# Kernel optimization log

Measured on AMD Instinct MI355X. Metric: run time of the kernel, lower is better.

Reference implementation:

```python
import jax, jax.numpy as jnp
import numpy as np

B = 2048          # number of trees (batch)
K = 511           # nodes per complete binary tree (depth 9: levels 0..8)
DEPTH = 9
VOCAB = 200000
EDIM = 128


def setup_inputs() -> dict:
    key = jax.random.key(0)
    k1, k2, k3, k4 = jax.random.split(key, 4)
    N = B * K
    i = np.arange(K)
    lvl = np.floor(np.log2(i + 1)).astype(np.int32)            # level within tree, 0..8
    par_local = np.where(i > 0, (i - 1) // 2, 0).astype(np.int64)  # root points to itself
    offs = (np.arange(B, dtype=np.int64) * K)[:, None]
    parent = jnp.asarray((offs + par_local[None, :]).reshape(-1), dtype=jnp.int32)
    level = jnp.asarray(np.tile(lvl, B), dtype=jnp.int32)
    batch_id = jnp.asarray(np.repeat(np.arange(B, dtype=np.int64), K), dtype=jnp.int32)
    tokens = jax.random.randint(k1, (N,), 0, VOCAB, dtype=jnp.int32)
    emb_weight = jax.random.normal(k2, (VOCAB, EDIM), dtype=jnp.float32) * 0.02
    W = jax.random.normal(k3, (EDIM, EDIM), dtype=jnp.float32) * 0.05
    b = jax.random.normal(k4, (EDIM,), dtype=jnp.float32) * 0.01
    return {"emb_weight": emb_weight, "W": W, "b": b,
            "tokens": tokens, "parent": parent, "level": level, "batch_id": batch_id}


def reference(emb_weight, W, b, tokens, parent, level, batch_id):
    # per-node projection: W_c(embedding(token))  -> [N, EDIM]
    h = emb_weight[tokens] @ W + b
    # bottom-up child aggregation: h[parent] += h[child], deepest level first
    for l in range(DEPTH - 1, 0, -1):
        contrib = jnp.where((level == l)[:, None], h, 0.0)
        h = h.at[parent].add(contrib)
    # torch.max over all node_list snapshots == per-tree elementwise max of node
    # states, clamped at 0 by the zero rows of untouched batch_node snapshots.
    seg_max = jax.ops.segment_max(h, batch_id, num_segments=B)
    return jnp.maximum(seg_max, 0.0)
```

## Files before the change

### kernel.cpp

```cpp
#include <hip/hip_runtime.h>
#include <hip/hip_bf16.h>
#include <stdint.h>

#define VOCAB 200000
#define EDIM 128
#define NTREES 2048
#define KNODES 511

typedef __attribute__((ext_vector_type(4))) float f32x4;
typedef __attribute__((ext_vector_type(2))) float f32x2;
typedef __attribute__((ext_vector_type(8))) short s16x8;
typedef __attribute__((ext_vector_type(8))) unsigned short u16x8;

__device__ __forceinline__ unsigned short f2bf(float x) {
  unsigned u = __builtin_bit_cast(unsigned, x);
  return (unsigned short)((u + 0x7fffu + ((u >> 16) & 1u)) >> 16);
}
__device__ __forceinline__ float bf2f(unsigned short h) {
  unsigned u = ((unsigned)h) << 16;
  return __builtin_bit_cast(float, u);
}

__device__ __forceinline__ unsigned fp8enc(float v) {
  unsigned u = __builtin_bit_cast(unsigned, v);
  unsigned s = (u >> 24) & 0x80u;
  unsigned au = u & 0x7fffffffu;
  au = au > 0x43E00000u ? 0x43E00000u : au;
  unsigned r = au + 0x0007ffffu + ((au >> 20) & 1u);
  unsigned code = (((r >> 23) - 120u) << 3) | ((r >> 20) & 7u);
  float a = __builtin_bit_cast(float, au);
  unsigned sub = (unsigned)(int)rintf(a * 512.0f);
  unsigned c = (au < 0x3C800000u) ? sub : code;
  return c | s;
}
__device__ __forceinline__ float fp8dec(unsigned b) {
  unsigned e = (b >> 3) & 15u, m = b & 7u;
  float n = __builtin_bit_cast(float, ((e + 120u) << 23) | (m << 20));
  float sv = (float)(int)m * 0.001953125f;
  float v = e ? n : sv;
  return (b & 0x80u) ? -v : v;
}

__device__ __forceinline__ unsigned enc4(float a, float b, float c, float d) {
#if __has_builtin(__builtin_amdgcn_cvt_pk_fp8_f32)
  int pk = 0;
  pk = __builtin_amdgcn_cvt_pk_fp8_f32(a, b, pk, false);
  pk = __builtin_amdgcn_cvt_pk_fp8_f32(c, d, pk, true);
  return (unsigned)pk;
#else
  return fp8enc(a) | (fp8enc(b) << 8) | (fp8enc(c) << 16) | (fp8enc(d) << 24);
#endif
}

__device__ __forceinline__ void dec8(uint2 v, float* o) {
#if __has_builtin(__builtin_amdgcn_cvt_pk_f32_fp8)
  f32x2 a = __builtin_amdgcn_cvt_pk_f32_fp8(v.x, false);
  f32x2 b = __builtin_amdgcn_cvt_pk_f32_fp8(v.x, true);
  f32x2 c = __builtin_amdgcn_cvt_pk_f32_fp8(v.y, false);
  f32x2 d = __builtin_amdgcn_cvt_pk_f32_fp8(v.y, true);
  o[0] = a[0]; o[1] = a[1]; o[2] = b[0]; o[3] = b[1];
  o[4] = c[0]; o[5] = c[1]; o[6] = d[0]; o[7] = d[1];
#else
#pragma unroll
  for (int i = 0; i < 4; ++i) o[i] = fp8dec((v.x >> (8 * i)) & 0xFFu);
#pragma unroll
  for (int i = 0; i < 4; ++i) o[4 + i] = fp8dec((v.y >> (8 * i)) & 0xFFu);
#endif
}

__device__ __forceinline__ s16x8 cvt8(f32x4 a, f32x4 b) {
  u16x8 t;
#pragma unroll
  for (int i = 0; i < 4; ++i)
    t[i] = __builtin_bit_cast(unsigned short, __float2bfloat16(a[i]));
#pragma unroll
  for (int i = 0; i < 4; ++i)
    t[4 + i] = __builtin_bit_cast(unsigned short, __float2bfloat16(b[i]));
  return __builtin_bit_cast(s16x8, t);
}

__global__ __launch_bounds__(256) void proj_kernel(
    const float* __restrict__ emb, const float* __restrict__ W,
    const float* __restrict__ bias, unsigned char* __restrict__ T8) {
  __shared__ unsigned short WT[EDIM][136];
  __shared__ float bsh[EDIM];

  const int tid = threadIdx.x;
  for (int idx = tid; idx < EDIM * EDIM; idx += 256) {
    int k = idx >> 7, n = idx & 127;
    WT[n][k] = f2bf(W[idx] * 64.0f);
  }
  if (tid < EDIM) bsh[tid] = bias[tid] * 64.0f;
  __syncthreads();

  const int w = tid >> 6, lane = tid & 63;
  const int q = lane >> 4, cl = lane & 15;
  const long rowbase = (long)blockIdx.x * 128 + (long)w * 32;

  const float* rowp[2];
#pragma unroll
  for (int rt = 0; rt < 2; ++rt) {
    long r = rowbase + rt * 16 + cl;
    if (r >= VOCAB) r = VOCAB - 1;
    rowp[rt] = emb + r * EDIM + q * 8;
  }

  f32x4 acc[2][8];
#pragma unroll
  for (int rt = 0; rt < 2; ++rt)
#pragma unroll
    for (int nt = 0; nt < 8; ++nt) acc[rt][nt] = (f32x4){0.f, 0.f, 0.f, 0.f};

  f32x4 pa[2][2], pb[2][2];
#pragma unroll
  for (int rt = 0; rt < 2; ++rt) {
    pa[0][rt] = *(const f32x4*)(rowp[rt]);
    pb[0][rt] = *(const f32x4*)(rowp[rt] + 4);
  }

#pragma unroll
  for (int ks = 0; ks < 4; ++ks) {
    const int cur = ks & 1, nxt = cur ^ 1;
    if (ks < 3) {
#pragma unroll
      for (int rt = 0; rt < 2; ++rt) {
        pa[nxt][rt] = *(const f32x4*)(rowp[rt] + (ks + 1) * 32);
        pb[nxt][rt] = *(const f32x4*)(rowp[rt] + (ks + 1) * 32 + 4);
      }
    }
    s16x8 ef[2];
#pragma unroll
    for (int rt = 0; rt < 2; ++rt) ef[rt] = cvt8(pa[cur][rt], pb[cur][rt]);

    const int k0 = ks * 32 + q * 8;
#pragma unroll
    for (int nt = 0; nt < 8; ++nt) {
      s16x8 wf = *(const s16x8*)&WT[nt * 16 + cl][k0];
#pragma unroll
      for (int rt = 0; rt < 2; ++rt)
        acc[rt][nt] = __builtin_amdgcn_mfma_f32_16x16x32_bf16(wf, ef[rt], acc[rt][nt], 0, 0, 0);
    }
  }

#pragma unroll
  for (int rt = 0; rt < 2; ++rt) {
    long row = rowbase + rt * 16 + cl;
    if (row < VOCAB) {
#pragma unroll
      for (int nt = 0; nt < 8; ++nt) {
        const int col0 = nt * 16 + q * 4;
        float g0 = acc[rt][nt][0] + bsh[col0 + 0];
        float g1 = acc[rt][nt][1] + bsh[col0 + 1];
        float g2 = acc[rt][nt][2] + bsh[col0 + 2];
        float g3 = acc[rt][nt][3] + bsh[col0 + 3];
        *(unsigned*)&T8[row * EDIM + col0] = enc4(g0, g1, g2, g3);
      }
    }
  }
}

__global__ __launch_bounds__(512, 4) void tree_kernel(
    const unsigned char* __restrict__ T8, const int* __restrict__ tokens,
    float* __restrict__ out) {
  __shared__ unsigned char P8[512][EDIM];
  unsigned char* lds = &P8[0][0];
  const int SOFF = 16384;
  const int MOFF = 53248;

  const int tid = threadIdx.x;
  const int tree = blockIdx.x;
  const int wv = tid >> 6, lane = tid & 63;

  const int* tk = tokens + (long)tree * KNODES;
  int toks[8];
#pragma unroll
  for (int i = 0; i < 8; ++i) {
    int node = wv * 64 + i * 8 + (lane >> 3);
    toks[i] = tk[node > 510 ? 510 : node];
  }
  const int chunk = (lane & 7) ^ ((lane >> 3) & 7);
#pragma unroll
  for (int i = 0; i < 8; ++i) {
    const unsigned char* src = T8 + (long)toks[i] * EDIM + chunk * 16;
    unsigned char* dst = &P8[wv * 64 + i * 8][0];
    __builtin_amdgcn_global_load_lds(
        (const __attribute__((address_space(1))) unsigned int*)src,
        (__attribute__((address_space(3))) unsigned int*)dst, 16, 0, 0);
  }
  __syncthreads();

  auto ldP8 = [&](int row, int q8) -> uint2 {
    int g = q8 >> 1, h = q8 & 1;
    return *(const uint2*)(lds + row * 128 + (((g ^ (row & 7))) << 4) + h * 8);
  };
  auto saddr = [&](int slot, int q16) -> unsigned char* {
    return lds + SOFF + slot * 288 + ((q16 ^ (slot & 7)) << 4);
  };

  const int q = tid & 15;
  const int jg = tid >> 4;
  float rmax[8];
#pragma unroll
  for (int e = 0; e < 8; ++e) rmax[e] = 0.f;

  u16x8 sp7[4];
#pragma unroll
  for (int k = 0; k < 4; ++k) {
    const int p = jg + 32 * k, m = 127 + p;
    uint2 pr = ldP8(m, q);
    uint2 xr = ldP8(2 * m + 1, q);
    uint2 yr = ldP8(2 * m + 2, q);
    float pv[8], xv[8], yv[8];
    dec8(pr, pv); dec8(xr, xv); dec8(yr, yv);
#pragma unroll
    for (int e = 0; e < 8; ++e) {
      float sv = pv[e] + xv[e] + yv[e];
      rmax[e] = fmaxf(rmax[e], fmaxf(fmaxf(xv[e], yv[e]), sv));
      sp7[k][e] = f2bf(sv);
    }
  }
  __syncthreads();
#pragma unroll
  for (int k = 0; k < 4; ++k) *(u16x8*)saddr(jg + 32 * k, q) = sp7[k];
  __syncthreads();

  for (int l = 6; l >= 0; --l) {
    const int cnt = 1 << l;
    for (int p = jg; p < cnt; p += 32) {
      const int m = cnt - 1 + p;
      const int ps = p << (7 - l);
      const int c2s = ps + (1 << (6 - l));
      uint2 pr = ldP8(m, q);
      u16x8 c1 = *(const u16x8*)saddr(ps, q);
      u16x8 c2 = *(const u16x8*)saddr(c2s, q);
      float pv[8];
      dec8(pr, pv);
      u16x8 sp;
#pragma unroll
      for (int e = 0; e < 8; ++e) {
        float sv = pv[e] + bf2f(c1[e]) + bf2f(c2[e]);
        rmax[e] = fmaxf(rmax[e], sv);
        sp[e] = f2bf(sv);
      }
      *(u16x8*)saddr(ps, q) = sp;
    }
    __syncthreads();
  }

#pragma unroll
  for (int e = 0; e < 8; ++e) {
    rmax[e] = fmaxf(rmax[e], __shfl_xor(rmax[e], 16, 64));
    rmax[e] = fmaxf(rmax[e], __shfl_xor(rmax[e], 32, 64));
  }
  float* mb = (float*)(lds + MOFF);
  if (lane < 16) {
#pragma unroll
    for (int e = 0; e < 8; ++e) mb[wv * 128 + lane * 8 + e] = rmax[e];
  }
  __syncthreads();
  if (tid < 128) {
    float v = mb[tid];
#pragma unroll
    for (int w2 = 1; w2 < 8; ++w2) v = fmaxf(v, mb[w2 * 128 + tid]);
    out[(long)tree * 128 + tid] = v * 0.015625f;
  }
}

extern "C" void kernel_launch(void* const* d_in, const int* in_sizes, int n_in,
                              void* d_out, int out_size, void* d_ws, size_t ws_size,
                              hipStream_t stream) {
  const float* emb = (const float*)d_in[0];
  const float* W = (const float*)d_in[1];
  const float* b = (const float*)d_in[2];
  const int* tokens = (const int*)d_in[3];

  unsigned char* T8 = (unsigned char*)d_ws;
  float* out = (float*)d_out;

  const int nblk1 = (VOCAB + 127) / 128;
  proj_kernel<<<nblk1, 256, 0, stream>>>(emb, W, b, T8);
  tree_kernel<<<NTREES, 512, 0, stream>>>(T8, tokens, out);
}
```

Before: 74.88 us.

## Precompute bf16 transposed W once, read it from global in projection kernel

Adds a small prep kernel that converts W to scaled bf16 in transposed layout, plus a scaled bias, both written to workspace. The projection kernel no longer fills an LDS copy of W or synchronises per block; it reads W fragments directly from global/L2 and initialises accumulators with the bias. It also prefetches two k-steps of embedding rows ahead instead of one. This removes the per-block W conversion and barrier across about 1563 blocks, at the cost of an extra launch and more global/L2 traffic for W fragments.

```diff
diff --git a/kernel.cpp b/kernel.cpp
--- a/kernel.cpp
+++ b/kernel.cpp
@@ -79,20 +79,21 @@
   return __builtin_bit_cast(s16x8, t);
 }
 
+__global__ __launch_bounds__(256) void wprep_kernel(
+    const float* __restrict__ W, const float* __restrict__ b,
+    unsigned short* __restrict__ WTb, float* __restrict__ bsc) {
+  int idx = blockIdx.x * 256 + threadIdx.x;
+  if (idx < EDIM * EDIM) {
+    int k = idx >> 7, n = idx & 127;
+    WTb[n * EDIM + k] = f2bf(W[idx] * 64.0f);
+  }
+  if (idx < EDIM) bsc[idx] = b[idx] * 64.0f;
+}
+
 __global__ __launch_bounds__(256) void proj_kernel(
-    const float* __restrict__ emb, const float* __restrict__ W,
-    const float* __restrict__ bias, unsigned char* __restrict__ T8) {
-  __shared__ unsigned short WT[EDIM][136];
-  __shared__ float bsh[EDIM];
-
+    const float* __restrict__ emb, const unsigned short* __restrict__ WTb,
+    const float* __restrict__ bsc, unsigned char* __restrict__ T8) {
   const int tid = threadIdx.x;
-  for (int idx = tid; idx < EDIM * EDIM; idx += 256) {
-    int k = idx >> 7, n = idx & 127;
-    WT[n][k] = f2bf(W[idx] * 64.0f);
-  }
-  if (tid < EDIM) bsh[tid] = bias[tid] * 64.0f;
-  __syncthreads();
-
   const int w = tid >> 6, lane = tid & 63;
   const int q = lane >> 4, cl = lane & 15;
   const long rowbase = (long)blockIdx.x * 128 + (long)w * 32;
@@ -107,38 +108,40 @@
 
   f32x4 acc[2][8];
 #pragma unroll
-  for (int rt = 0; rt < 2; ++rt)
-#pragma unroll
-    for (int nt = 0; nt < 8; ++nt) acc[rt][nt] = (f32x4){0.f, 0.f, 0.f, 0.f};
-
-  f32x4 pa[2][2], pb[2][2];
-#pragma unroll
-  for (int rt = 0; rt < 2; ++rt) {
-    pa[0][rt] = *(const f32x4*)(rowp[rt]);
-    pb[0][rt] = *(const f32x4*)(rowp[rt] + 4);
-  }
+  for (int nt = 0; nt < 8; ++nt) {
+    f32x4 bv = *(const f32x4*)(bsc + nt * 16 + q * 4);
+    acc[0][nt] = bv;
+    acc[1][nt] = bv;
+  }
+
+  f32x4 ea[4][2], eb[4][2];
+#pragma unroll
+  for (int ks = 0; ks < 2; ++ks)
+#pragma unroll
+    for (int rt = 0; rt < 2; ++rt) {
+      ea[ks][rt] = *(const f32x4*)(rowp[rt] + ks * 32);
+      eb[ks][rt] = *(const f32x4*)(rowp[rt] + ks * 32 + 4);
+    }
 
 #pragma unroll
   for (int ks = 0; ks < 4; ++ks) {
-    const int cur = ks & 1, nxt = cur ^ 1;
-    if (ks < 3) {
+    if (ks < 2) {
 #pragma unroll
       for (int rt = 0; rt < 2; ++rt) {
-        pa[nxt][rt] = *(const f32x4*)(rowp[rt] + (ks + 1) * 32);
-        pb[nxt][rt] = *(const f32x4*)(rowp[rt] + (ks + 1) * 32 + 4);
+        ea[ks + 2][rt] = *(const f32x4*)(rowp[rt] + (ks + 2) * 32);
+        eb[ks + 2][rt] = *(const f32x4*)(rowp[rt] + (ks + 2) * 32 + 4);
       }
     }
     s16x8 ef[2];
 #pragma unroll
-    for (int rt = 0; rt < 2; ++rt) ef[rt] = cvt8(pa[cur][rt], pb[cur][rt]);
-
-    const int k0 = ks * 32 + q * 8;
+    for (int rt = 0; rt < 2; ++rt) ef[rt] = cvt8(ea[ks][rt], eb[ks][rt]);
+
+    const unsigned short* wbase = WTb + ks * 32 + q * 8;
 #pragma unroll
     for (int nt = 0; nt < 8; ++nt) {
-      s16x8 wf = *(const s16x8*)&WT[nt * 16 + cl][k0];
-#pragma unroll
-      for (int rt = 0; rt < 2; ++rt)
-        acc[rt][nt] = __builtin_amdgcn_mfma_f32_16x16x32_bf16(wf, ef[rt], acc[rt][nt], 0, 0, 0);
+      s16x8 wf = *(const s16x8*)(wbase + (nt * 16 + cl) * EDIM);
+      acc[0][nt] = __builtin_amdgcn_mfma_f32_16x16x32_bf16(wf, ef[0], acc[0][nt], 0, 0, 0);
+      acc[1][nt] = __builtin_amdgcn_mfma_f32_16x16x32_bf16(wf, ef[1], acc[1][nt], 0, 0, 0);
     }
   }
 
@@ -149,11 +152,8 @@
 #pragma unroll
       for (int nt = 0; nt < 8; ++nt) {
         const int col0 = nt * 16 + q * 4;
-        float g0 = acc[rt][nt][0] + bsh[col0 + 0];
-        float g1 = acc[rt][nt][1] + bsh[col0 + 1];
-        float g2 = acc[rt][nt][2] + bsh[col0 + 2];
-        float g3 = acc[rt][nt][3] + bsh[col0 + 3];
-        *(unsigned*)&T8[row * EDIM + col0] = enc4(g0, g1, g2, g3);
+        *(unsigned*)&T8[row * EDIM + col0] =
+            enc4(acc[rt][nt][0], acc[rt][nt][1], acc[rt][nt][2], acc[rt][nt][3]);
       }
     }
   }
@@ -275,9 +275,12 @@
   const int* tokens = (const int*)d_in[3];
 
   unsigned char* T8 = (unsigned char*)d_ws;
+  unsigned short* WTb = (unsigned short*)((char*)d_ws + 25600000);
+  float* bsc = (float*)((char*)d_ws + 25632768);
   float* out = (float*)d_out;
 
+  wprep_kernel<<<64, 256, 0, stream>>>(W, b, WTb, bsc);
   const int nblk1 = (VOCAB + 127) / 128;
-  proj_kernel<<<nblk1, 256, 0, stream>>>(emb, W, b, T8);
+  proj_kernel<<<nblk1, 256, 0, stream>>>(emb, WTb, bsc, T8);
   tree_kernel<<<NTREES, 512, 0, stream>>>(T8, tokens, out);
 }
```

New measurement: 93.69 us. +25.1%, slower.
